# Optimization experiments

Measured on AMD Instinct MI355X. Metric: run time of the kernel, lower is better.

## Reference

```python
import jax, jax.numpy as jnp
import numpy as np

D_MODEL = 512
NUM_HEADS = 8
D_K = D_MODEL // NUM_HEADS


def setup_inputs() -> dict:
    key = jax.random.key(0)
    ks = jax.random.split(key, 12)
    B, Sq, Sk = 4, 2048, 2048
    scale = 1.0 / np.sqrt(D_MODEL)
    inp = {
        'query': jax.random.normal(ks[0], (B, Sq, D_MODEL), jnp.float32),
        'key':   jax.random.normal(ks[1], (B, Sk, D_MODEL), jnp.float32),
        'value': jax.random.normal(ks[2], (B, Sk, D_MODEL), jnp.float32),
        'wq': jax.random.normal(ks[3], (D_MODEL, D_MODEL), jnp.float32) * scale,
        'bq': jnp.zeros((D_MODEL,), jnp.float32),
        'wk': jax.random.normal(ks[4], (D_MODEL, D_MODEL), jnp.float32) * scale,
        'bk': jnp.zeros((D_MODEL,), jnp.float32),
        'wv': jax.random.normal(ks[5], (D_MODEL, D_MODEL), jnp.float32) * scale,
        'bv': jnp.zeros((D_MODEL,), jnp.float32),
        'wo': jax.random.normal(ks[6], (D_MODEL, D_MODEL), jnp.float32) * scale,
        'bo': jnp.zeros((D_MODEL,), jnp.float32),
        'ln_g': jnp.ones((D_MODEL,), jnp.float32),
        'ln_b': jnp.zeros((D_MODEL,), jnp.float32),
    }
    return inp


def _layer_norm(x, g, b, eps=1e-5):
    mu = jnp.mean(x, axis=-1, keepdims=True)
    var = jnp.mean(jnp.square(x - mu), axis=-1, keepdims=True)
    return (x - mu) * jax.lax.rsqrt(var + eps) * g + b


def reference(query, key, value, wq, bq, wk, bk, wv, bv, wo, bo, ln_g, ln_b):
    B, Sq, _ = query.shape
    Sk = key.shape[1]
    residual = query
    # projections: torch Linear computes x @ W^T + b; here wq is (out,in)-free:
    # we store weights as (d_model, d_model) and use x @ W + b (equivalent param space)
    Q = (query @ wq + bq).reshape(B, Sq, NUM_HEADS, D_K).transpose(0, 2, 1, 3)
    K = (key   @ wk + bk).reshape(B, Sk, NUM_HEADS, D_K).transpose(0, 2, 1, 3)
    V = (value @ wv + bv).reshape(B, Sk, NUM_HEADS, D_K).transpose(0, 2, 1, 3)
    scores = jnp.einsum('bhqd,bhkd->bhqk', Q, K) / jnp.sqrt(jnp.float32(D_K))
    attn = jax.nn.softmax(scores, axis=-1)  # dropout is identity in eval
    context = jnp.einsum('bhqk,bhkd->bhqd', attn, V)
    context = context.transpose(0, 2, 1, 3).reshape(B, Sq, D_MODEL)
    out = context @ wo + bo
    return _layer_norm(out + residual, ln_g, ln_b)
```

## Files before the change

kernel.cpp:

```cpp
#include <hip/hip_runtime.h>
#include <cstdint>
#include <cstddef>

typedef unsigned short u16;
typedef __bf16 bf16x8 __attribute__((ext_vector_type(8)));
typedef __bf16 bf16x4 __attribute__((ext_vector_type(4)));
typedef float f32x4 __attribute__((ext_vector_type(4)));

#define DEVI __device__ __forceinline__

DEVI u16 f2bf(float f){
  union { float f; unsigned u; } v; v.f = f;
  unsigned r = v.u + 0x7fffu + ((v.u >> 16) & 1u);
  return (u16)(r >> 16);
}

#if defined(__has_builtin)
#if __has_builtin(__builtin_amdgcn_exp2f)
#define EXP2F(x) __builtin_amdgcn_exp2f(x)
#else
#define EXP2F(x) exp2f(x)
#endif
#else
#define EXP2F(x) exp2f(x)
#endif

#define MFMA16(a,b,c) __builtin_amdgcn_mfma_f32_16x16x32_bf16((a),(b),(c),0,0,0)

DEVI void gload_lds16(const void* g, void* l){
  __builtin_amdgcn_global_load_lds(
      (const __attribute__((address_space(1))) void*)g,
      (__attribute__((address_space(3))) void*)l, 16, 0, 0);
}

#define BARRIER do{ __builtin_amdgcn_s_barrier(); \
    __builtin_amdgcn_sched_barrier(0); }while(0)


__global__ void k_prep_x(const float* __restrict__ q, const float* __restrict__ k,
                         const float* __restrict__ v, u16* __restrict__ xb){
  size_t t = (size_t)blockIdx.x*blockDim.x + threadIdx.x;
  size_t base = t*8;
  const float* s;
  if (base < 4194304u)      s = q + base;
  else if (base < 8388608u) s = k + (base - 4194304u);
  else                      s = v + (base - 8388608u);
  float4 a = *(const float4*)s;
  float4 b = *(const float4*)(s+4);
  ushort4 o0, o1;
  o0.x=f2bf(a.x); o0.y=f2bf(a.y); o0.z=f2bf(a.z); o0.w=f2bf(a.w);
  o1.x=f2bf(b.x); o1.y=f2bf(b.y); o1.z=f2bf(b.z); o1.w=f2bf(b.w);
  *(ushort4*)(xb + base)     = o0;
  *(ushort4*)(xb + base + 4) = o1;
}

__global__ void k_prep_w(const float* __restrict__ w0, const float* __restrict__ w1,
                         const float* __restrict__ w2, const float* __restrict__ w3,
                         u16* __restrict__ wt){
  __shared__ u16 tile[64][72];
  int p = blockIdx.z;
  const float* W = (p==0)?w0:((p==1)?w1:((p==2)?w2:w3));
  int k0 = blockIdx.x*64, n0 = blockIdx.y*64;
  int t = threadIdx.x;
  int tr = t >> 4, tc = t & 15;
  #pragma unroll
  for (int pass=0; pass<4; pass++){
    int row = pass*16 + tr;
    float4 a = *(const float4*)(W + (size_t)(k0+row)*512 + n0 + tc*4);
    tile[row][tc*4+0] = f2bf(a.x);
    tile[row][tc*4+1] = f2bf(a.y);
    tile[row][tc*4+2] = f2bf(a.z);
    tile[row][tc*4+3] = f2bf(a.w);
  }
  __syncthreads();
  #pragma unroll
  for (int pass=0; pass<4; pass++){
    int n = pass*16 + tr;
    ushort4 o;
    o.x = tile[tc*4+0][n];
    o.y = tile[tc*4+1][n];
    o.z = tile[tc*4+2][n];
    o.w = tile[tc*4+3][n];
    *(ushort4*)(wt + (size_t)p*262144 + (size_t)(n0+n)*512 + k0 + tc*4) = o;
  }
}

__global__ __launch_bounds__(256)
void k_gemm_qkv(const u16* __restrict__ xb, const u16* __restrict__ wt,
                const float* __restrict__ bq, const float* __restrict__ bk,
                const float* __restrict__ bv,
                u16* __restrict__ qb, u16* __restrict__ kb, u16* __restrict__ vt){
  int l = threadIdx.x & 63, w = threadIdx.x >> 6;
  int lr = l & 15, lg = l >> 4;
  int f = blockIdx.x;
  int xcd = f & 7, j0 = f >> 3;
  int pm   = xcd*24 + (j0 >> 2);
  int nblk = j0 & 3;
  int p    = pm >> 6, mblk = pm & 63;
  int wr = w >> 1, wc = w & 1;

  const float* bias = (p==0)?bq:((p==1)?bk:bv);
  float osc = (p==0)? (0.125f*1.44269504088896340736f) : 1.0f;

  const char* Ag = (const char*)(xb + (size_t)p*4194304 + (size_t)mblk*128*512);
  const char* Bg = (const char*)(wt + (size_t)p*262144  + (size_t)nblk*128*512);

  __shared__ __align__(16) u16 Albuf[2][8192];
  __shared__ __align__(16) u16 Blbuf[2][8192];

  int r8 = l >> 3, sl = l & 7;

  #define STAGE_G(t, buf) do{ \
    _Pragma("unroll") \
    for (int cc=0; cc<4; ++cc){ \
      int c = w*4 + cc; int row = c*8 + r8; \
      int sw = (sl ^ (row & 7)) << 4; \
      gload_lds16(Ag + (size_t)row*1024 + (size_t)(t)*128 + sw, (char*)Albuf[buf] + c*1024); \
      gload_lds16(Bg + (size_t)row*1024 + (size_t)(t)*128 + sw, (char*)Blbuf[buf] + c*1024); \
    } }while(0)

  STAGE_G(0, 0);

  f32x4 acc[4][4] = {};
  for (int t = 0; t < 8; ++t){
    int cur = t & 1;
    if (t < 7){
      STAGE_G(t+1, cur^1);
      asm volatile("s_waitcnt vmcnt(8)" ::: "memory");
    } else {
      asm volatile("s_waitcnt vmcnt(0)" ::: "memory");
    }
    BARRIER;
    const char* Ac = (const char*)Albuf[cur];
    const char* Bc = (const char*)Blbuf[cur];
    #pragma unroll
    for (int kk=0;kk<2;kk++){
      int ks = ((kk*4 + lg) ^ (lr & 7)) << 4;
      bf16x8 af[4], bfr[4];
      #pragma unroll
      for (int i=0;i<4;i++)
        af[i]  = *(const bf16x8*)(Ac + (wr*64 + i*16 + lr)*128 + ks);
      #pragma unroll
      for (int j=0;j<4;j++)
        bfr[j] = *(const bf16x8*)(Bc + (wc*64 + j*16 + lr)*128 + ks);
      #pragma unroll
      for (int i=0;i<4;i++)
        #pragma unroll
        for (int j=0;j<4;j++)
          acc[i][j] = MFMA16(af[i], bfr[j], acc[i][j]);
    }
    if (t < 7) BARRIER;
  }
  #undef STAGE_G

  int m0 = mblk*128 + wr*64;
  int n0 = nblk*128 + wc*64;
  if (p < 2){
    u16* outp = (p==0)?qb:kb;
    #pragma unroll
    for (int i=0;i<4;i++){
      #pragma unroll
      for (int j=0;j<4;j++){
        int n = n0 + j*16 + lr;
        int h = n >> 6, d = n & 63;
        float bb = bias[n];
        #pragma unroll
        for (int rg=0;rg<4;rg++){
          int m = m0 + i*16 + 4*lg + rg;
          int b = m >> 11, s = m & 2047;
          float val = (acc[i][j][rg] + bb)*osc;
          __bf16 hb = (__bf16)val;
          outp[(((size_t)b*8 + h)*2048 + s)*64 + d] = *(u16*)&hb;
        }
      }
    }
  } else {
    #pragma unroll
    for (int i=0;i<4;i++){
      #pragma unroll
      for (int j=0;j<4;j++){
        int n = n0 + j*16 + lr;
        int h = n >> 6, d = n & 63;
        float bb = bias[n];
        int m = m0 + i*16 + 4*lg;
        int b = m >> 11, s = m & 2047;
        ushort4 o;
        #pragma unroll
        for (int rg=0;rg<4;rg++){
          __bf16 hb = (__bf16)(acc[i][j][rg] + bb);
          ((u16*)&o)[rg] = *(u16*)&hb;
        }
        *(ushort4*)(vt + (((size_t)(b*8+h)*64 + d)*2048 + s)) = o;
      }
    }
  }
}

__global__ __launch_bounds__(512, 4)
void k_attn(const u16* __restrict__ qbuf, const u16* __restrict__ kbuf,
            const u16* __restrict__ vtb, u16* __restrict__ opart,
            float* __restrict__ lpart){
  int l = threadIdx.x & 63, w = threadIdx.x >> 6;
  int lr = l & 15, lg = l >> 4;
  int f = blockIdx.x;
  int bh    = (f & 7)*4 + ((f >> 3) & 3);
  int rest  = f >> 5;
  int split = rest & 1;
  int q0    = (rest >> 1)*256 + w*32;
  int b = bh >> 3, h = bh & 7;
  int kvbase = split*1024;

  const u16* Qp = qbuf + ((size_t)bh*2048 + q0)*64;
  const char* Kg = (const char*)(kbuf + (size_t)bh*2048*64) + (size_t)kvbase*128;
  const char* Vg = (const char*)(vtb  + (size_t)bh*64*2048) + (size_t)kvbase*2;

  __shared__ __align__(16) u16 Klds[2][4096];
  __shared__ __align__(16) u16 Vlds[2][4096];
  __shared__ __align__(16) u16 Plds[8][2048];
  u16* Pw = Plds[w];

  int r8 = l >> 3, sl = l & 7;

  bf16x8 qf[2][2];
  #pragma unroll
  for (int j=0;j<2;j++)
    #pragma unroll
    for (int kk=0;kk<2;kk++)
      qf[j][kk] = *(const bf16x8*)(Qp + (size_t)(j*16+lr)*64 + kk*32 + lg*8);

  {
    int row = w*8 + r8;
    int sw = (sl ^ (row & 7)) << 4;
    gload_lds16(Kg + (size_t)row*128 + sw,  (char*)Klds[0] + w*1024);
    gload_lds16(Vg + (size_t)row*4096 + sw, (char*)Vlds[0] + w*1024);
  }

  f32x4 oacc[2][4] = {};
  float lsum[2] = {0.f, 0.f};
  const float M = 16.0f;

  for (int t = 0; t < 16; ++t){
    int cur = t & 1;
    if (t < 15){
      int row = w*8 + r8;
      int sw = (sl ^ (row & 7)) << 4;
      gload_lds16(Kg + (size_t)(t+1)*8192 + (size_t)row*128 + sw,
                  (char*)Klds[cur^1] + w*1024);
      gload_lds16(Vg + (size_t)(t+1)*128 + (size_t)row*4096 + sw,
                  (char*)Vlds[cur^1] + w*1024);
      asm volatile("s_waitcnt vmcnt(2)" ::: "memory");
    } else {
      asm volatile("s_waitcnt vmcnt(0)" ::: "memory");
    }
    BARRIER;
    const char* Kc = (const char*)Klds[cur];
    const char* Vc = (const char*)Vlds[cur];
    f32x4 sacc[4][2] = {};
    #pragma unroll
    for (int kk=0;kk<2;kk++){
      bf16x8 kf[4];
      #pragma unroll
      for (int i=0;i<4;i++)
        kf[i] = *(const bf16x8*)(Kc + (i*16+lr)*128 + (((4*kk+lg)^(lr&7))<<4));
      #pragma unroll
      for (int i=0;i<4;i++)
        #pragma unroll
        for (int j=0;j<2;j++)
          sacc[i][j] = MFMA16(kf[i], qf[j][kk], sacc[i][j]);
    }
    #pragma unroll
    for (int j=0;j<2;j++){
      int qrow = lr + 16*j;
      #pragma unroll
      for (int i=0;i<4;i++){
        bf16x4 pk;
        #pragma unroll
        for (int rg=0;rg<4;rg++){
          float pv = EXP2F(sacc[i][j][rg] - M);
          lsum[j] += pv;
          pk[rg] = (__bf16)pv;
        }
        int o    = 8*lg + 32*i;
        int slot = (o >> 4) ^ (qrow & 7);
        *(bf16x4*)((char*)Pw + qrow*128 + (slot<<4) + (o & 15)) = pk;
      }
    }
    #pragma unroll
    for (int kk=0;kk<2;kk++){
      bf16x8 pf[2];
      #pragma unroll
      for (int fi=0;fi<2;fi++){
        int qrow = fi*16 + lr;
        int slot = (4*kk + lg) ^ (qrow & 7);
        pf[fi] = *(const bf16x8*)((char*)Pw + qrow*128 + (slot<<4));
      }
      bf16x8 vf[4];
      #pragma unroll
      for (int fj=0;fj<4;fj++)
        vf[fj] = *(const bf16x8*)(Vc + (fj*16+lr)*128 + (((4*kk+lg)^(lr&7))<<4));
      #pragma unroll
      for (int fi=0;fi<2;fi++)
        #pragma unroll
        for (int fj=0;fj<4;fj++)
          oacc[fi][fj] = MFMA16(pf[fi], vf[fj], oacc[fi][fj]);
    }
    if (t < 15) BARRIER;
  }

  #pragma unroll
  for (int j=0;j<2;j++){
    lsum[j] += __shfl_xor(lsum[j], 16);
    lsum[j] += __shfl_xor(lsum[j], 32);
  }
  if (lg == 0){
    #pragma unroll
    for (int j=0;j<2;j++)
      lpart[((size_t)split*32 + bh)*2048 + q0 + 16*j + lr] = lsum[j];
  }
  u16* op = opart + (size_t)split*8192*512;
  #pragma unroll
  for (int fi=0;fi<2;fi++){
    #pragma unroll
    for (int fj=0;fj<4;fj++){
      int col = h*64 + fj*16 + lr;
      #pragma unroll
      for (int rg=0;rg<4;rg++){
        int qg = q0 + fi*16 + 4*lg + rg;
        __bf16 hb = (__bf16)oacc[fi][fj][rg];
        op[((size_t)(b*2048 + qg))*512 + col] = *(u16*)&hb;
      }
    }
  }
}

__global__ __launch_bounds__(256)
void k_gemm_o(const u16* __restrict__ op0, const u16* __restrict__ op1,
              const float* __restrict__ lpart, const u16* __restrict__ wto,
              u16* __restrict__ gout){
  int l = threadIdx.x & 63, w = threadIdx.x >> 6;
  int lr = l & 15, lg = l >> 4;
  int f = blockIdx.x;
  int xcd = f & 7, j0 = f >> 3;
  int mblk = xcd*16 + (j0 >> 2);
  int nblk = j0 & 3;
  int wr = w & 1, wc = w >> 1;

  int bb8 = (mblk >> 5) * 8;
  int qbase = (mblk & 31) * 64;

  const u16* Ag0 = op0 + (size_t)mblk*64*512;
  const u16* Ag1 = op1 + (size_t)mblk*64*512;
  const char* Bg = (const char*)(wto + (size_t)nblk*128*512);

  __shared__ __align__(16) u16 Albuf[2][4096];
  __shared__ __align__(16) u16 Blbuf[2][8192];

  int r8 = l >> 3, sl = l & 7;

  bf16x8 a0v[2], a1v[2]; float l0v[2], l1v[2];
  #define A_ISSUE(tt) do{ \
    _Pragma("unroll") \
    for (int cc=0; cc<2; ++cc){ \
      int c = w*2 + cc; int row = c*8 + r8; \
      int ssrc = sl ^ (row & 7); \
      a0v[cc] = *(const bf16x8*)(Ag0 + (size_t)row*512 + (tt)*64 + ssrc*8); \
      a1v[cc] = *(const bf16x8*)(Ag1 + (size_t)row*512 + (tt)*64 + ssrc*8); \
      int q = qbase + row; \
      l0v[cc] = lpart[(size_t)(bb8 + (tt))*2048 + q]; \
      l1v[cc] = lpart[(size_t)(32 + bb8 + (tt))*2048 + q]; \
    } }while(0)

  #define A_WRITE(buf) do{ \
    _Pragma("unroll") \
    for (int cc=0; cc<2; ++cc){ \
      int c = w*2 + cc; \
      float inv = 1.f / (l0v[cc] + l1v[cc]); \
      bf16x8 r; \
      _Pragma("unroll") \
      for (int e=0;e<8;e++) \
        r[e] = (__bf16)(((float)a0v[cc][e] + (float)a1v[cc][e]) * inv); \
      *(bf16x8*)((char*)Albuf[buf] + c*1024 + r8*128 + sl*16) = r; \
    } }while(0)

  #define B_STAGE(tt, buf) do{ \
    _Pragma("unroll") \
    for (int cc=0; cc<4; ++cc){ \
      int c = w*4 + cc; int row = c*8 + r8; \
      int sw = (sl ^ (row & 7)) << 4; \
      gload_lds16(Bg + (size_t)row*1024 + (size_t)(tt)*128 + sw, (char*)Blbuf[buf] + c*1024); \
    } }while(0)

  A_ISSUE(0);
  B_STAGE(0, 0);
  asm volatile("s_waitcnt vmcnt(4)" ::: "memory");
  A_WRITE(0);
  asm volatile("s_waitcnt lgkmcnt(0)" ::: "memory");

  f32x4 acc[2][4] = {};
  for (int t = 0; t < 8; ++t){
    int cur = t & 1;
    if (t < 7){
      A_ISSUE(t+1);
      B_STAGE(t+1, cur^1);
      asm volatile("s_waitcnt vmcnt(12)" ::: "memory");
    } else {
      asm volatile("s_waitcnt vmcnt(0)" ::: "memory");
    }
    BARRIER;
    const char* Ac = (const char*)Albuf[cur];
    const char* Bc = (const char*)Blbuf[cur];
    #pragma unroll
    for (int kk=0;kk<2;kk++){
      int ks = ((kk*4 + lg) ^ (lr & 7)) << 4;
      bf16x8 af[2], bfr[4];
      #pragma unroll
      for (int i=0;i<2;i++)
        af[i]  = *(const bf16x8*)(Ac + (wr*32 + i*16 + lr)*128 + ks);
      #pragma unroll
      for (int j=0;j<4;j++)
        bfr[j] = *(const bf16x8*)(Bc + (wc*64 + j*16 + lr)*128 + ks);
      #pragma unroll
      for (int i=0;i<2;i++)
        #pragma unroll
        for (int j=0;j<4;j++)
          acc[i][j] = MFMA16(af[i], bfr[j], acc[i][j]);
    }
    if (t < 7){
      asm volatile("s_waitcnt vmcnt(4)" ::: "memory");
      A_WRITE(cur^1);
      asm volatile("s_waitcnt lgkmcnt(0)" ::: "memory");
      BARRIER;
    }
  }
  #undef A_ISSUE
  #undef A_WRITE
  #undef B_STAGE

  int m0 = mblk*64 + wr*32;
  int n0 = nblk*128 + wc*64;
  #pragma unroll
  for (int i=0;i<2;i++){
    #pragma unroll
    for (int j=0;j<4;j++){
      int n = n0 + j*16 + lr;
      #pragma unroll
      for (int rg=0;rg<4;rg++){
        int m = m0 + i*16 + 4*lg + rg;
        __bf16 hb = (__bf16)acc[i][j][rg];
        gout[(size_t)m*512 + n] = *(u16*)&hb;
      }
    }
  }
}

__global__ __launch_bounds__(256)
void k_ln(const u16* __restrict__ gout, const float* __restrict__ bo,
          const float* __restrict__ resid, const float* __restrict__ g,
          const float* __restrict__ beta, float* __restrict__ out){
  int gid  = blockIdx.x*256 + threadIdx.x;
  int row  = gid >> 6;
  int lane = gid & 63;
  int c0 = lane*8;
  bf16x8 a = *(const bf16x8*)(gout + (size_t)row*512 + c0);
  float4 r0 = *(const float4*)(resid + (size_t)row*512 + c0);
  float4 r1 = *(const float4*)(resid + (size_t)row*512 + c0 + 4);
  float4 b0 = *(const float4*)(bo + c0);
  float4 b1 = *(const float4*)(bo + c0 + 4);
  float v[8];
  v[0]=(float)a[0]+b0.x+r0.x; v[1]=(float)a[1]+b0.y+r0.y;
  v[2]=(float)a[2]+b0.z+r0.z; v[3]=(float)a[3]+b0.w+r0.w;
  v[4]=(float)a[4]+b1.x+r1.x; v[5]=(float)a[5]+b1.y+r1.y;
  v[6]=(float)a[6]+b1.z+r1.z; v[7]=(float)a[7]+b1.w+r1.w;
  float s1 = 0.f, s2 = 0.f;
  #pragma unroll
  for (int e=0;e<8;e++){ s1 += v[e]; s2 += v[e]*v[e]; }
  #pragma unroll
  for (int mk=1; mk<64; mk<<=1){
    s1 += __shfl_xor(s1, mk);
    s2 += __shfl_xor(s2, mk);
  }
  float mu   = s1 * (1.f/512.f);
  float var  = s2 * (1.f/512.f) - mu*mu;
  float rstd = rsqrtf(var + 1e-5f);
  float4 g0 = *(const float4*)(g + c0);
  float4 g1 = *(const float4*)(g + c0 + 4);
  float4 e0 = *(const float4*)(beta + c0);
  float4 e1 = *(const float4*)(beta + c0 + 4);
  float4 o0, o1;
  o0.x=(v[0]-mu)*rstd*g0.x+e0.x; o0.y=(v[1]-mu)*rstd*g0.y+e0.y;
  o0.z=(v[2]-mu)*rstd*g0.z+e0.z; o0.w=(v[3]-mu)*rstd*g0.w+e0.w;
  o1.x=(v[4]-mu)*rstd*g1.x+e1.x; o1.y=(v[5]-mu)*rstd*g1.y+e1.y;
  o1.z=(v[6]-mu)*rstd*g1.z+e1.z; o1.w=(v[7]-mu)*rstd*g1.w+e1.w;
  *(float4*)(out + (size_t)row*512 + c0)     = o0;
  *(float4*)(out + (size_t)row*512 + c0 + 4) = o1;
}

extern "C" void kernel_launch(void* const* d_in, const int* in_sizes, int n_in,
                              void* d_out, int out_size, void* d_ws, size_t ws_size,
                              hipStream_t stream){
  const float* q   = (const float*)d_in[0];
  const float* k   = (const float*)d_in[1];
  const float* v   = (const float*)d_in[2];
  const float* wq  = (const float*)d_in[3];
  const float* bq  = (const float*)d_in[4];
  const float* wk  = (const float*)d_in[5];
  const float* bk  = (const float*)d_in[6];
  const float* wv  = (const float*)d_in[7];
  const float* bv  = (const float*)d_in[8];
  const float* wo  = (const float*)d_in[9];
  const float* bo  = (const float*)d_in[10];
  const float* lng = (const float*)d_in[11];
  const float* lnb = (const float*)d_in[12];
  float* out = (float*)d_out;
  char* ws = (char*)d_ws;
  u16*   xb    = (u16*)(ws + 0);
  u16*   opart = (u16*)(ws + 0);
  float* lpart = (float*)(ws + 16777216);
  u16*   wt    = (u16*)(ws + 25165824);
  u16*   qb    = (u16*)(ws + 27262976);
  u16*   kb    = (u16*)(ws + 35651584);
  u16*   vt    = (u16*)(ws + 44040192);
  u16*   gout  = (u16*)(ws + 52428800);

  k_prep_x<<<6144, 256, 0, stream>>>(q, k, v, xb);
  k_prep_w<<<dim3(8,8,4), 256, 0, stream>>>(wq, wk, wv, wo, wt);
  k_gemm_qkv<<<768, 256, 0, stream>>>(xb, wt, bq, bk, bv, qb, kb, vt);
  k_attn<<<512, 512, 0, stream>>>(qb, kb, vt, opart, lpart);
  k_gemm_o<<<512, 256, 0, stream>>>(opart, opart + (size_t)8192*512, lpart,
                                    wt + 3*262144, gout);
  k_ln<<<2048, 256, 0, stream>>>(gout, bo, q, lng, lnb, out);
}
```

Measured before the change: 102.7 us.

## Split attention KV into three chunks and halve per-wave P staging LDS

The attention kernel now splits the 2048-key range into three partial chunks (704/704/640 keys) instead of two, launching 768 blocks rather than 512. The output-projection GEMM merges three partial outputs and three row sums. The P tile in LDS is halved by writing and consuming one 16-row half at a time, so occupancy can rise to 6 blocks per CU under the new launch bounds. The cost is an extra partial buffer to write and read, a third load stream in the GEMM, and the workspace layout is reshuffled to fit it.

```diff
diff --git a/kernel.cpp b/kernel.cpp
--- a/kernel.cpp
+++ b/kernel.cpp
@@ -196,7 +196,7 @@
   }
 }
 
-__global__ __launch_bounds__(512, 4)
+__global__ __launch_bounds__(512, 6)
 void k_attn(const u16* __restrict__ qbuf, const u16* __restrict__ kbuf,
             const u16* __restrict__ vtb, u16* __restrict__ opart,
             float* __restrict__ lpart){
@@ -205,10 +205,12 @@
   int f = blockIdx.x;
   int bh    = (f & 7)*4 + ((f >> 3) & 3);
   int rest  = f >> 5;
-  int split = rest & 1;
-  int q0    = (rest >> 1)*256 + w*32;
+  int split = rest % 3;
+  int qt    = rest / 3;
+  int q0    = qt*256 + w*32;
   int b = bh >> 3, h = bh & 7;
-  int kvbase = split*1024;
+  int kvbase = split*704;
+  int nt     = (split < 2) ? 11 : 10;
 
   const u16* Qp = qbuf + ((size_t)bh*2048 + q0)*64;
   const char* Kg = (const char*)(kbuf + (size_t)bh*2048*64) + (size_t)kvbase*128;
@@ -216,7 +218,7 @@
 
   __shared__ __align__(16) u16 Klds[2][4096];
   __shared__ __align__(16) u16 Vlds[2][4096];
-  __shared__ __align__(16) u16 Plds[8][2048];
+  __shared__ __align__(16) u16 Plds[8][1024];
   u16* Pw = Plds[w];
 
   int r8 = l >> 3, sl = l & 7;
@@ -239,9 +241,9 @@
   float lsum[2] = {0.f, 0.f};
   const float M = 16.0f;
 
-  for (int t = 0; t < 16; ++t){
+  for (int t = 0; t < nt; ++t){
     int cur = t & 1;
-    if (t < 15){
+    if (t < nt-1){
       int row = w*8 + r8;
       int sw = (sl ^ (row & 7)) << 4;
       gload_lds16(Kg + (size_t)(t+1)*8192 + (size_t)row*128 + sw,
@@ -270,7 +272,10 @@
     }
     #pragma unroll
     for (int j=0;j<2;j++){
-      int qrow = lr + 16*j;
+      if (j == 1){
+        asm volatile("s_waitcnt lgkmcnt(0)" ::: "memory");
+        __builtin_amdgcn_sched_barrier(0);
+      }
       #pragma unroll
       for (int i=0;i<4;i++){
         bf16x4 pk;
@@ -281,30 +286,23 @@
           pk[rg] = (__bf16)pv;
         }
         int o    = 8*lg + 32*i;
-        int slot = (o >> 4) ^ (qrow & 7);
-        *(bf16x4*)((char*)Pw + qrow*128 + (slot<<4) + (o & 15)) = pk;
-      }
-    }
-    #pragma unroll
-    for (int kk=0;kk<2;kk++){
-      bf16x8 pf[2];
-      #pragma unroll
-      for (int fi=0;fi<2;fi++){
-        int qrow = fi*16 + lr;
-        int slot = (4*kk + lg) ^ (qrow & 7);
-        pf[fi] = *(const bf16x8*)((char*)Pw + qrow*128 + (slot<<4));
-      }
-      bf16x8 vf[4];
-      #pragma unroll
-      for (int fj=0;fj<4;fj++)
-        vf[fj] = *(const bf16x8*)(Vc + (fj*16+lr)*128 + (((4*kk+lg)^(lr&7))<<4));
-      #pragma unroll
-      for (int fi=0;fi<2;fi++)
+        int slot = (o >> 4) ^ (lr & 7);
+        *(bf16x4*)((char*)Pw + lr*128 + (slot<<4) + (o & 15)) = pk;
+      }
+      #pragma unroll
+      for (int kk=0;kk<2;kk++){
+        int slot = (4*kk + lg) ^ (lr & 7);
+        bf16x8 pf = *(const bf16x8*)((char*)Pw + lr*128 + (slot<<4));
+        bf16x8 vf[4];
         #pragma unroll
         for (int fj=0;fj<4;fj++)
-          oacc[fi][fj] = MFMA16(pf[fi], vf[fj], oacc[fi][fj]);
-    }
-    if (t < 15) BARRIER;
+          vf[fj] = *(const bf16x8*)(Vc + (fj*16+lr)*128 + (((4*kk+lg)^(lr&7))<<4));
+        #pragma unroll
+        for (int fj=0;fj<4;fj++)
+          oacc[j][fj] = MFMA16(pf, vf[fj], oacc[j][fj]);
+      }
+    }
+    if (t < nt-1) BARRIER;
   }
 
   #pragma unroll
@@ -335,8 +333,8 @@
 
 __global__ __launch_bounds__(256)
 void k_gemm_o(const u16* __restrict__ op0, const u16* __restrict__ op1,
-              const float* __restrict__ lpart, const u16* __restrict__ wto,
-              u16* __restrict__ gout){
+              const u16* __restrict__ op2, const float* __restrict__ lpart,
+              const u16* __restrict__ wto, u16* __restrict__ gout){
   int l = threadIdx.x & 63, w = threadIdx.x >> 6;
   int lr = l & 15, lg = l >> 4;
   int f = blockIdx.x;
@@ -350,6 +348,7 @@
 
   const u16* Ag0 = op0 + (size_t)mblk*64*512;
   const u16* Ag1 = op1 + (size_t)mblk*64*512;
+  const u16* Ag2 = op2 + (size_t)mblk*64*512;
   const char* Bg = (const char*)(wto + (size_t)nblk*128*512);
 
   __shared__ __align__(16) u16 Albuf[2][4096];
@@ -357,7 +356,7 @@
 
   int r8 = l >> 3, sl = l & 7;
 
-  bf16x8 a0v[2], a1v[2]; float l0v[2], l1v[2];
+  bf16x8 a0v[2], a1v[2], a2v[2]; float l0v[2], l1v[2], l2v[2];
   #define A_ISSUE(tt) do{ \
     _Pragma("unroll") \
     for (int cc=0; cc<2; ++cc){ \
@@ -365,20 +364,22 @@
       int ssrc = sl ^ (row & 7); \
       a0v[cc] = *(const bf16x8*)(Ag0 + (size_t)row*512 + (tt)*64 + ssrc*8); \
       a1v[cc] = *(const bf16x8*)(Ag1 + (size_t)row*512 + (tt)*64 + ssrc*8); \
+      a2v[cc] = *(const bf16x8*)(Ag2 + (size_t)row*512 + (tt)*64 + ssrc*8); \
       int q = qbase + row; \
       l0v[cc] = lpart[(size_t)(bb8 + (tt))*2048 + q]; \
       l1v[cc] = lpart[(size_t)(32 + bb8 + (tt))*2048 + q]; \
+      l2v[cc] = lpart[(size_t)(64 + bb8 + (tt))*2048 + q]; \
     } }while(0)
 
   #define A_WRITE(buf) do{ \
     _Pragma("unroll") \
     for (int cc=0; cc<2; ++cc){ \
       int c = w*2 + cc; \
-      float inv = 1.f / (l0v[cc] + l1v[cc]); \
+      float inv = 1.f / (l0v[cc] + l1v[cc] + l2v[cc]); \
       bf16x8 r; \
       _Pragma("unroll") \
       for (int e=0;e<8;e++) \
-        r[e] = (__bf16)(((float)a0v[cc][e] + (float)a1v[cc][e]) * inv); \
+        r[e] = (__bf16)(((float)a0v[cc][e] + (float)a1v[cc][e] + (float)a2v[cc][e]) * inv); \
       *(bf16x8*)((char*)Albuf[buf] + c*1024 + r8*128 + sl*16) = r; \
     } }while(0)
 
@@ -402,7 +403,7 @@
     if (t < 7){
       A_ISSUE(t+1);
       B_STAGE(t+1, cur^1);
-      asm volatile("s_waitcnt vmcnt(12)" ::: "memory");
+      asm volatile("s_waitcnt vmcnt(16)" ::: "memory");
     } else {
       asm volatile("s_waitcnt vmcnt(0)" ::: "memory");
     }
@@ -513,20 +514,22 @@
   const float* lnb = (const float*)d_in[12];
   float* out = (float*)d_out;
   char* ws = (char*)d_ws;
-  u16*   xb    = (u16*)(ws + 0);
-  u16*   opart = (u16*)(ws + 0);
-  float* lpart = (float*)(ws + 16777216);
-  u16*   wt    = (u16*)(ws + 25165824);
-  u16*   qb    = (u16*)(ws + 27262976);
-  u16*   kb    = (u16*)(ws + 35651584);
-  u16*   vt    = (u16*)(ws + 44040192);
-  u16*   gout  = (u16*)(ws + 52428800);
+  u16*   wt    = (u16*)(ws + 0);
+  u16*   qb    = (u16*)(ws + 2097152);
+  u16*   kb    = (u16*)(ws + 10485760);
+  u16*   vt    = (u16*)(ws + 18874368);
+  u16*   gout  = (u16*)(ws + 27262976);
+  u16*   xb    = (u16*)(ws + 35651584);
+  u16*   opart = (u16*)(ws + 35651584);
+  float* lpart = (float*)(ws + 60817408);
 
   k_prep_x<<<6144, 256, 0, stream>>>(q, k, v, xb);
   k_prep_w<<<dim3(8,8,4), 256, 0, stream>>>(wq, wk, wv, wo, wt);
   k_gemm_qkv<<<768, 256, 0, stream>>>(xb, wt, bq, bk, bv, qb, kb, vt);
-  k_attn<<<512, 512, 0, stream>>>(qb, kb, vt, opart, lpart);
-  k_gemm_o<<<512, 256, 0, stream>>>(opart, opart + (size_t)8192*512, lpart,
-                                    wt + 3*262144, gout);
+  k_attn<<<768, 512, 0, stream>>>(qb, kb, vt, opart, lpart);
+  k_gemm_o<<<512, 256, 0, stream>>>(opart,
+                                    opart + (size_t)8192*512,
+                                    opart + (size_t)2*8192*512,
+                                    lpart, wt + 3*262144, gout);
   k_ln<<<2048, 256, 0, stream>>>(gout, bo, q, lng, lnb, out);
 }
```

Result: slower. 364.1 us (+254.4%).

## Fuse fp32-to-bf16 activation conversion into QKV GEMM A-tile loading

Applied to the files above, without the earlier changes.

Removes the separate k_prep_x kernel that converted query/key/value to bf16 in a workspace buffer. The QKV GEMM now loads fp32 A tiles into registers, converts them to bf16 and writes them swizzled into LDS, double-buffered against the asynchronous B loads. This saves a kernel launch and a full write-then-read pass over 24 MB of bf16 intermediate data. In exchange, the GEMM reads twice as many A bytes per tile, uses extra registers, and replaces direct global-to-LDS A copies with a manual register path and extra waitcnts. The workspace layout is rearranged to match.

```diff
diff --git a/kernel.cpp b/kernel.cpp
--- a/kernel.cpp
+++ b/kernel.cpp
@@ -37,23 +37,6 @@
     __builtin_amdgcn_sched_barrier(0); }while(0)
 
 
-__global__ void k_prep_x(const float* __restrict__ q, const float* __restrict__ k,
-                         const float* __restrict__ v, u16* __restrict__ xb){
-  size_t t = (size_t)blockIdx.x*blockDim.x + threadIdx.x;
-  size_t base = t*8;
-  const float* s;
-  if (base < 4194304u)      s = q + base;
-  else if (base < 8388608u) s = k + (base - 4194304u);
-  else                      s = v + (base - 8388608u);
-  float4 a = *(const float4*)s;
-  float4 b = *(const float4*)(s+4);
-  ushort4 o0, o1;
-  o0.x=f2bf(a.x); o0.y=f2bf(a.y); o0.z=f2bf(a.z); o0.w=f2bf(a.w);
-  o1.x=f2bf(b.x); o1.y=f2bf(b.y); o1.z=f2bf(b.z); o1.w=f2bf(b.w);
-  *(ushort4*)(xb + base)     = o0;
-  *(ushort4*)(xb + base + 4) = o1;
-}
-
 __global__ void k_prep_w(const float* __restrict__ w0, const float* __restrict__ w1,
                          const float* __restrict__ w2, const float* __restrict__ w3,
                          u16* __restrict__ wt){
@@ -86,7 +69,8 @@
 }
 
 __global__ __launch_bounds__(256)
-void k_gemm_qkv(const u16* __restrict__ xb, const u16* __restrict__ wt,
+void k_gemm_qkv(const float* __restrict__ xq, const float* __restrict__ xk,
+                const float* __restrict__ xv, const u16* __restrict__ wt,
                 const float* __restrict__ bq, const float* __restrict__ bk,
                 const float* __restrict__ bv,
                 u16* __restrict__ qb, u16* __restrict__ kb, u16* __restrict__ vt){
@@ -102,31 +86,59 @@
   const float* bias = (p==0)?bq:((p==1)?bk:bv);
   float osc = (p==0)? (0.125f*1.44269504088896340736f) : 1.0f;
 
-  const char* Ag = (const char*)(xb + (size_t)p*4194304 + (size_t)mblk*128*512);
-  const char* Bg = (const char*)(wt + (size_t)p*262144  + (size_t)nblk*128*512);
+  const float* Ag32 = ((p==0)?xq:((p==1)?xk:xv)) + (size_t)mblk*128*512;
+  const char*  Bg   = (const char*)(wt + (size_t)p*262144 + (size_t)nblk*128*512);
 
   __shared__ __align__(16) u16 Albuf[2][8192];
   __shared__ __align__(16) u16 Blbuf[2][8192];
 
   int r8 = l >> 3, sl = l & 7;
-
-  #define STAGE_G(t, buf) do{ \
+  int ar = w*8 + r8;
+  int as = sl;
+
+  float4 av[8];
+  #define A_ISSUE(tt) do{ \
+    _Pragma("unroll") \
+    for (int p4=0; p4<4; ++p4){ \
+      int r = ar + p4*32; \
+      const float* src = Ag32 + (size_t)r*512 + (tt)*64 + as*8; \
+      av[p4*2]   = *(const float4*)src; \
+      av[p4*2+1] = *(const float4*)(src+4); \
+    } }while(0)
+
+  #define A_WRITE(buf) do{ \
+    _Pragma("unroll") \
+    for (int p4=0; p4<4; ++p4){ \
+      int r = ar + p4*32; \
+      bf16x8 o; \
+      o[0]=(__bf16)av[p4*2].x;   o[1]=(__bf16)av[p4*2].y; \
+      o[2]=(__bf16)av[p4*2].z;   o[3]=(__bf16)av[p4*2].w; \
+      o[4]=(__bf16)av[p4*2+1].x; o[5]=(__bf16)av[p4*2+1].y; \
+      o[6]=(__bf16)av[p4*2+1].z; o[7]=(__bf16)av[p4*2+1].w; \
+      *(bf16x8*)((char*)Albuf[buf] + r*128 + ((as ^ (r & 7)) << 4)) = o; \
+    } }while(0)
+
+  #define B_STAGE(tt, buf) do{ \
     _Pragma("unroll") \
     for (int cc=0; cc<4; ++cc){ \
       int c = w*4 + cc; int row = c*8 + r8; \
       int sw = (sl ^ (row & 7)) << 4; \
-      gload_lds16(Ag + (size_t)row*1024 + (size_t)(t)*128 + sw, (char*)Albuf[buf] + c*1024); \
-      gload_lds16(Bg + (size_t)row*1024 + (size_t)(t)*128 + sw, (char*)Blbuf[buf] + c*1024); \
+      gload_lds16(Bg + (size_t)row*1024 + (size_t)(tt)*128 + sw, (char*)Blbuf[buf] + c*1024); \
     } }while(0)
 
-  STAGE_G(0, 0);
+  A_ISSUE(0);
+  B_STAGE(0, 0);
+  asm volatile("s_waitcnt vmcnt(4)" ::: "memory");
+  A_WRITE(0);
+  asm volatile("s_waitcnt lgkmcnt(0)" ::: "memory");
 
   f32x4 acc[4][4] = {};
   for (int t = 0; t < 8; ++t){
     int cur = t & 1;
     if (t < 7){
-      STAGE_G(t+1, cur^1);
-      asm volatile("s_waitcnt vmcnt(8)" ::: "memory");
+      A_ISSUE(t+1);
+      B_STAGE(t+1, cur^1);
+      asm volatile("s_waitcnt vmcnt(12)" ::: "memory");
     } else {
       asm volatile("s_waitcnt vmcnt(0)" ::: "memory");
     }
@@ -149,9 +161,16 @@
         for (int j=0;j<4;j++)
           acc[i][j] = MFMA16(af[i], bfr[j], acc[i][j]);
     }
-    if (t < 7) BARRIER;
-  }
-  #undef STAGE_G
+    if (t < 7){
+      asm volatile("s_waitcnt vmcnt(4)" ::: "memory");
+      A_WRITE(cur^1);
+      asm volatile("s_waitcnt lgkmcnt(0)" ::: "memory");
+      BARRIER;
+    }
+  }
+  #undef A_ISSUE
+  #undef A_WRITE
+  #undef B_STAGE
 
   int m0 = mblk*128 + wr*64;
   int n0 = nblk*128 + wc*64;
@@ -513,18 +532,16 @@
   const float* lnb = (const float*)d_in[12];
   float* out = (float*)d_out;
   char* ws = (char*)d_ws;
-  u16*   xb    = (u16*)(ws + 0);
-  u16*   opart = (u16*)(ws + 0);
-  float* lpart = (float*)(ws + 16777216);
-  u16*   wt    = (u16*)(ws + 25165824);
-  u16*   qb    = (u16*)(ws + 27262976);
-  u16*   kb    = (u16*)(ws + 35651584);
-  u16*   vt    = (u16*)(ws + 44040192);
-  u16*   gout  = (u16*)(ws + 52428800);
-
-  k_prep_x<<<6144, 256, 0, stream>>>(q, k, v, xb);
+  u16*   wt    = (u16*)(ws + 0);
+  u16*   qb    = (u16*)(ws + 2097152);
+  u16*   kb    = (u16*)(ws + 10485760);
+  u16*   vt    = (u16*)(ws + 18874368);
+  u16*   gout  = (u16*)(ws + 27262976);
+  u16*   opart = (u16*)(ws + 35651584);
+  float* lpart = (float*)(ws + 52428800);
+
   k_prep_w<<<dim3(8,8,4), 256, 0, stream>>>(wq, wk, wv, wo, wt);
-  k_gemm_qkv<<<768, 256, 0, stream>>>(xb, wt, bq, bk, bv, qb, kb, vt);
+  k_gemm_qkv<<<768, 256, 0, stream>>>(q, k, v, wt, bq, bk, bv, qb, kb, vt);
   k_attn<<<512, 512, 0, stream>>>(qb, kb, vt, opart, lpart);
   k_gemm_o<<<512, 256, 0, stream>>>(opart, opart + (size_t)8192*512, lpart,
                                     wt + 3*262144, gout);
```

Result: no change. 101.1 us (-1.6%).
